# Kernel optimization log

Hardware: AMD Instinct MI355X
Metric: run time of the kernel (lower is better)

## Reference

```python
import jax, jax.numpy as jnp
import numpy as np

# Dimensions (see shape_source)
L = 1024   # episode_len (memory slots)
B = 64     # batch (parallel envs)
K = 512    # key_size
V = 512    # value_size
H = 8      # num_head
MEMB = 256 # memory_state_embedding
SDIM = 512 # state_dim
HID = 512  # hidden width of all 2-layer encoders
RIMQ = 512 # rim_query_size
LAT = K - MEMB  # task_inference_latent dim


def setup_inputs() -> dict:
    key = jax.random.key(0)
    ks = jax.random.split(key, 16)
    w = lambda k, shape: (jax.random.normal(k, shape, jnp.float32) * 0.02)
    return {
        "state": jax.random.normal(ks[0], (B, SDIM), jnp.float32),
        "task_inference_latent": jax.random.normal(ks[1], (B, LAT), jnp.float32),
        "keys": jax.random.normal(ks[2], (L, B, K), jnp.float32),
        "vals": jax.random.normal(ks[3], (L, B, V), jnp.float32),
        "rpe_mod": jax.random.uniform(ks[4], (L, B, 1), jnp.float32),
        "step": jnp.maximum(jax.random.randint(ks[5], (B,), 0, L), 1),
        "W_state": w(ks[6], (SDIM, MEMB)), "b_state": jnp.zeros((MEMB,), jnp.float32),
        "Wcq1": w(ks[7], (K, HID)), "bcq1": jnp.zeros((HID,), jnp.float32),
        "Wcq2": w(ks[8], (HID, K)), "bcq2": jnp.zeros((K,), jnp.float32),
        "Wq": w(ks[9], (K, H * K)), "bq": jnp.zeros((H * K,), jnp.float32),
        "Wagg": w(ks[10], (H * V, V)), "bagg": jnp.zeros((V,), jnp.float32),
        "Wrk1": w(ks[11], (V, HID)), "brk1": jnp.zeros((HID,), jnp.float32),
        "Wrk2": w(ks[12], (HID, RIMQ)), "brk2": jnp.zeros((RIMQ,), jnp.float32),
        "Wrv1": w(ks[13], (V, HID)), "brv1": jnp.zeros((HID,), jnp.float32),
        "Wrv2": w(ks[14], (HID, V)), "brv2": jnp.zeros((V,), jnp.float32),
    }


def reference(state, task_inference_latent, keys, vals, rpe_mod, step,
              W_state, b_state, Wcq1, bcq1, Wcq2, bcq2, Wq, bq, Wagg, bagg,
              Wrk1, brk1, Wrk2, brk2, Wrv1, brv1, Wrv2, brv2):
    # DND.read (exploration branch), vectorized over the batch loop.
    se = state @ W_state + b_state                         # state_encoder: [B, MEMB]
    q = jnp.concatenate([se, task_inference_latent], -1)   # [B, K]
    # concat_query_encoder: stacked Linears with NO nonlinearity (faithful to source)
    q = (q @ Wcq1 + bcq1) @ Wcq2 + bcq2                    # [B, K]
    q = (q @ Wq + bq).reshape(B, H, K)                     # multi-head queries

    mk = keys * rpe_mod                                    # RPE-modulated keys [L, B, K]
    scores = jnp.einsum('lbk,bhk->blh', mk, q) / jnp.sqrt(jnp.float32(K))  # [B, L, H]
    valid = jnp.arange(L)[None, :] < step[:, None]         # [B, L] only slots < step[i]
    scores = jnp.where(valid[:, :, None], scores, jnp.float32(-1e30))
    prob = jax.nn.softmax(scores, axis=1) * valid[:, :, None].astype(scores.dtype)

    result = jnp.einsum('blh,lbv->bhv', prob, vals).reshape(B, H * V)
    result = (result @ Wagg + bagg)[:, None, :]            # value_aggregator -> [B, 1, V]
    out_key = (result @ Wrk1 + brk1) @ Wrk2 + brk2         # read_memory_to_key  [B, 1, RIMQ]
    out_val = (result @ Wrv1 + brv1) @ Wrv2 + brv2         # read_memory_to_value [B, 1, V]
    return out_key, out_val
```

## Files before the change

kernel.cpp:

```cpp
#include <hip/hip_runtime.h>
#include <math.h>

#define F4(p)  (*reinterpret_cast<float4*>(p))
#define CF4(p) (*reinterpret_cast<const float4*>(p))

#define NCHUNK 16

__device__ __forceinline__ void gemm_core(
    const float* __restrict__ Asrc, const float* __restrict__ inbias,
    const float* __restrict__ til,
    int NS, int srcld, int kc, int k0,
    const float* __restrict__ W, int ldw, int n0,
    const float* __restrict__ obias, float* __restrict__ Pout, int ldo)
{
    __shared__ float As[16*64], Ws[16*64];
    const int t = threadIdx.x;
    const int tx = t & 15, ty = t >> 4;
    const int row = t >> 2, kq = (t & 3) * 4;
    const int wrow = t >> 4, wcol = (t & 15) * 4;
    float acc[4][4] = {};
    for (int kk = 0; kk < kc; kk += 16) {
        const int kg = k0 + kk + kq;
        float4 av;
        if (til && kg >= 256) {
            av = CF4(&til[row*256 + (kg - 256)]);
        } else {
            av = {0.f, 0.f, 0.f, 0.f};
            if (inbias) av = CF4(&inbias[kg]);
            for (int s = 0; s < NS; ++s) {
                float4 v = CF4(&Asrc[(size_t)(s*64 + row)*srcld + kg]);
                av.x += v.x; av.y += v.y; av.z += v.z; av.w += v.w;
            }
        }
        As[(kq+0)*64+row] = av.x; As[(kq+1)*64+row] = av.y;
        As[(kq+2)*64+row] = av.z; As[(kq+3)*64+row] = av.w;
        F4(&Ws[wrow*64 + wcol]) = CF4(&W[(size_t)(k0 + kk + wrow)*ldw + n0 + wcol]);
        __syncthreads();
        #pragma unroll
        for (int k = 0; k < 16; ++k) {
            float4 a4 = CF4(&As[k*64 + ty*4]);
            float4 w4 = CF4(&Ws[k*64 + tx*4]);
            float a[4] = {a4.x, a4.y, a4.z, a4.w};
            float w[4] = {w4.x, w4.y, w4.z, w4.w};
            #pragma unroll
            for (int i = 0; i < 4; ++i)
                #pragma unroll
                for (int j = 0; j < 4; ++j)
                    acc[i][j] += a[i] * w[j];
        }
        __syncthreads();
    }
    #pragma unroll
    for (int i = 0; i < 4; ++i) {
        float4 o = {acc[i][0], acc[i][1], acc[i][2], acc[i][3]};
        if (obias) {
            float4 ob = CF4(&obias[n0 + tx*4]);
            o.x += ob.x; o.y += ob.y; o.z += ob.z; o.w += ob.w;
        }
        F4(&Pout[(size_t)(ty*4 + i)*ldo + n0 + tx*4]) = o;
    }
}

__global__ __launch_bounds__(256) void k_q1(
    const float* __restrict__ state, const float* __restrict__ W_state,
    float* __restrict__ P1)
{
    const int nt = blockIdx.x, ks = blockIdx.y;
    gemm_core(state, nullptr, nullptr, 1, 512, 64, ks*64,
              W_state, 256, nt*64, nullptr, P1 + (size_t)ks*64*256, 256);
}

__global__ __launch_bounds__(256) void k_q2(
    const float* __restrict__ P1, const float* __restrict__ b_state,
    const float* __restrict__ til, const float* __restrict__ Wcq1,
    float* __restrict__ P2)
{
    const int nt = blockIdx.x, ks = blockIdx.y;
    gemm_core(P1, b_state, til, 8, 256, 64, ks*64,
              Wcq1, 512, nt*64, nullptr, P2 + (size_t)ks*64*512, 512);
}

__global__ __launch_bounds__(256) void k_q3(
    const float* __restrict__ P2, const float* __restrict__ bcq1,
    const float* __restrict__ Wcq2, float* __restrict__ P3)
{
    const int nt = blockIdx.x, ks = blockIdx.y;
    gemm_core(P2, bcq1, nullptr, 8, 512, 64, ks*64,
              Wcq2, 512, nt*64, nullptr, P3 + (size_t)ks*64*512, 512);
}

__global__ __launch_bounds__(256) void k_qh(
    const float* __restrict__ P3, const float* __restrict__ bcq2,
    const float* __restrict__ Wq, float* __restrict__ P4)
{
    const int nt = blockIdx.x, ks = blockIdx.y;
    gemm_core(P3, bcq2, nullptr, 8, 512, 128, ks*128,
              Wq, 4096, nt*64, nullptr, P4 + (size_t)ks*64*4096, 4096);
}

__global__ __launch_bounds__(256) void k_qsum(
    const float* __restrict__ P4, const float* __restrict__ bq,
    float* __restrict__ qh)
{
    const int b = blockIdx.x, t = threadIdx.x;
    #pragma unroll
    for (int j = 0; j < 4; ++j) {
        int f = t + j*256;
        float4 v = CF4(&bq[f*4]);
        #pragma unroll
        for (int s = 0; s < 4; ++s) {
            float4 u = CF4(&P4[(size_t)(s*64 + b)*4096 + f*4]);
            v.x += u.x; v.y += u.y; v.z += u.z; v.w += u.w;
        }
        F4(&qh[(size_t)b*4096 + f*4]) = v;
    }
}

__global__ __launch_bounds__(256, 3) void k_fa(
    const float* __restrict__ keys, const float* __restrict__ rpe,
    const float* __restrict__ qh, const float* __restrict__ vals,
    const int* __restrict__ step,
    float* __restrict__ Facc, float* __restrict__ Fms)
{
    __shared__ float s_cmb[4096];
    __shared__ float s_sc[64*8];
    __shared__ float s_rpe[64];
    __shared__ float red[256];
    __shared__ float s_m[8];
    const int b = blockIdx.y, lc = blockIdx.x;
    const int sb = step[b];
    const int l0 = (lc * sb) / NCHUNK;
    const int l1 = ((lc + 1) * sb) / NCHUNK;
    const int nl = l1 - l0;
    const int t = threadIdx.x;
    float* facc_out = Facc + ((size_t)(lc*64) + b)*4096;
    if (nl <= 0) {
        float4 z = {0.f, 0.f, 0.f, 0.f};
        for (int i = t; i < 1024; i += 256) F4(&facc_out[i*4]) = z;
        if (t < 8) {
            size_t o = ((size_t)(lc*64 + b)*8 + t)*2;
            Fms[o] = -1e30f; Fms[o+1] = 0.f;
        }
        return;
    }
    const float inv_sqrtK = 0.04419417382415922f;
    if (t < nl) s_rpe[t] = rpe[(l0 + t)*64 + b] * inv_sqrtK;
    __syncthreads();

    const int lane = t & 63, w = t >> 6;
    float qr[8][8];
    {
        const float* qb = qh + (size_t)b*4096 + lane*8;
        #pragma unroll
        for (int h = 0; h < 8; ++h) {
            float4 x = CF4(&qb[h*512]);
            float4 y = CF4(&qb[h*512 + 4]);
            qr[h][0]=x.x; qr[h][1]=x.y; qr[h][2]=x.z; qr[h][3]=x.w;
            qr[h][4]=y.x; qr[h][5]=y.y; qr[h][6]=y.z; qr[h][7]=y.w;
        }
    }
    const bool p0 = lane & 1, p1 = lane & 2, p2 = lane & 4;
    const size_t RS = (size_t)64*512;

    const float* kbase = keys + ((size_t)l0*64 + b)*512 + lane*8;
    auto kaddr = [&](int r) { return kbase + (size_t)min(r, nl-1)*RS; };
    float4 kx0 = CF4(kaddr(w)),      ky0 = CF4(kaddr(w)+4);
    float4 kx1 = CF4(kaddr(w+4)),    ky1 = CF4(kaddr(w+4)+4);
    float4 kx2 = CF4(kaddr(w+8)),    ky2 = CF4(kaddr(w+8)+4);
    float4 kx3 = CF4(kaddr(w+12)),   ky3 = CF4(kaddr(w+12)+4);

    auto score_step = [&](float4& bx, float4& by, int r) {
        float kv[8] = {bx.x,bx.y,bx.z,bx.w, by.x,by.y,by.z,by.w};
        bx = CF4(kaddr(r+16)); by = CF4(kaddr(r+16)+4);
        float pr[8] = {};
        #pragma unroll
        for (int h = 0; h < 8; ++h)
            #pragma unroll
            for (int j = 0; j < 8; ++j)
                pr[h] += kv[j] * qr[h][j];
        float w4[4], x2[2], y;
        #pragma unroll
        for (int q = 0; q < 4; ++q) {
            float keep = p0 ? pr[2*q+1] : pr[2*q];
            float send = p0 ? pr[2*q]   : pr[2*q+1];
            w4[q] = keep + __shfl_xor(send, 1);
        }
        #pragma unroll
        for (int q = 0; q < 2; ++q) {
            float keep = p1 ? w4[2*q+1] : w4[2*q];
            float send = p1 ? w4[2*q]   : w4[2*q+1];
            x2[q] = keep + __shfl_xor(send, 2);
        }
        {
            float keep = p2 ? x2[1] : x2[0];
            float send = p2 ? x2[0] : x2[1];
            y = keep + __shfl_xor(send, 4);
        }
        y += __shfl_xor(y, 8);
        y += __shfl_xor(y, 16);
        y += __shfl_xor(y, 32);
        if (r < nl && lane < 8) s_sc[r*8 + lane] = y * s_rpe[r];
    };
    for (int il = w; il < nl; il += 16) {
        score_step(kx0, ky0, il);
        score_step(kx1, ky1, il + 4);
        score_step(kx2, ky2, il + 8);
        score_step(kx3, ky3, il + 12);
    }
    __syncthreads();

    const int h = t & 7, g = t >> 3;
    float m = -1e30f;
    for (int l = g; l < nl; l += 32) m = fmaxf(m, s_sc[l*8 + h]);
    red[g*8 + h] = m;
    __syncthreads();
    #pragma unroll
    for (int s = 16; s; s >>= 1) {
        if (g < s) red[g*8+h] = fmaxf(red[g*8+h], red[(g+s)*8+h]);
        __syncthreads();
    }
    if (t < 8) s_m[t] = red[t];
    __syncthreads();
    float mh = s_m[h], s_acc = 0.f;
    for (int l = g; l < nl; l += 32) {
        float e = __expf(s_sc[l*8 + h] - mh);
        s_sc[l*8 + h] = e;
        s_acc += e;
    }
    for (int l = nl + g; l < 64; l += 32) s_sc[l*8 + h] = 0.f;
    red[g*8 + h] = s_acc;
    __syncthreads();
    #pragma unroll
    for (int s = 16; s; s >>= 1) {
        if (g < s) red[g*8+h] += red[(g+s)*8+h];
        __syncthreads();
    }
    if (t < 8) {
        size_t o = ((size_t)(lc*64 + b)*8 + t)*2;
        Fms[o] = s_m[t]; Fms[o+1] = red[t];
    }
    __syncthreads();

    const int par = t >> 7, c = t & 127;
    float4 acc[8] = {};
    const float* vbase = vals + ((size_t)l0*64 + b)*512 + c*4;
    auto vaddr = [&](int r) { return vbase + (size_t)min(r, nl-1)*RS; };
    float4 v0 = CF4(vaddr(par));
    float4 v1 = CF4(vaddr(par+2));
    float4 v2 = CF4(vaddr(par+4));
    float4 v3 = CF4(vaddr(par+6));
    auto pv_step = [&](float4& vb, int row) {
        float4 v = vb;
        vb = CF4(vaddr(row + 8));
        float4 pa = CF4(&s_sc[row*8]);
        float4 pb = CF4(&s_sc[row*8 + 4]);
        acc[0].x += pa.x*v.x; acc[0].y += pa.x*v.y; acc[0].z += pa.x*v.z; acc[0].w += pa.x*v.w;
        acc[1].x += pa.y*v.x; acc[1].y += pa.y*v.y; acc[1].z += pa.y*v.z; acc[1].w += pa.y*v.w;
        acc[2].x += pa.z*v.x; acc[2].y += pa.z*v.y; acc[2].z += pa.z*v.z; acc[2].w += pa.z*v.w;
        acc[3].x += pa.w*v.x; acc[3].y += pa.w*v.y; acc[3].z += pa.w*v.z; acc[3].w += pa.w*v.w;
        acc[4].x += pb.x*v.x; acc[4].y += pb.x*v.y; acc[4].z += pb.x*v.z; acc[4].w += pb.x*v.w;
        acc[5].x += pb.y*v.x; acc[5].y += pb.y*v.y; acc[5].z += pb.y*v.z; acc[5].w += pb.y*v.w;
        acc[6].x += pb.z*v.x; acc[6].y += pb.z*v.y; acc[6].z += pb.z*v.z; acc[6].w += pb.z*v.w;
        acc[7].x += pb.w*v.x; acc[7].y += pb.w*v.y; acc[7].z += pb.w*v.z; acc[7].w += pb.w*v.w;
    };
    const int NL8 = (nl + 7) & ~7;
    for (int il = par; il < NL8; il += 8) {
        pv_step(v0, il);
        pv_step(v1, il + 2);
        pv_step(v2, il + 4);
        pv_step(v3, il + 6);
    }
    __syncthreads();
    if (par == 1) {
        #pragma unroll
        for (int hh = 0; hh < 8; ++hh)
            F4(&s_cmb[(c*8 + hh)*4]) = acc[hh];
    }
    __syncthreads();
    if (par == 0) {
        #pragma unroll
        for (int hh = 0; hh < 8; ++hh) {
            float4 o = CF4(&s_cmb[(c*8 + hh)*4]);
            o.x += acc[hh].x; o.y += acc[hh].y; o.z += acc[hh].z; o.w += acc[hh].w;
            F4(&facc_out[hh*512 + c*4]) = o;
        }
    }
}

__global__ __launch_bounds__(256) void k_comb(
    const float* __restrict__ Facc, const float* __restrict__ Fms,
    float* __restrict__ res)
{
    __shared__ float wgt[NCHUNK*8];
    const int b = blockIdx.x, t = threadIdx.x;
    if (t < 8) {
        float mm[NCHUNK], ss[NCHUNK], e[NCHUNK];
        float M = -1e30f;
        #pragma unroll
        for (int i = 0; i < NCHUNK; ++i) {
            size_t o = ((size_t)(i*64 + b)*8 + t)*2;
            mm[i] = Fms[o]; ss[i] = Fms[o+1];
            M = fmaxf(M, mm[i]);
        }
        float D = 0.f;
        #pragma unroll
        for (int i = 0; i < NCHUNK; ++i) { e[i] = __expf(mm[i] - M); D += e[i]*ss[i]; }
        float invD = 1.f / D;
        #pragma unroll
        for (int i = 0; i < NCHUNK; ++i) wgt[i*8 + t] = e[i] * invD;
    }
    __syncthreads();
    #pragma unroll
    for (int j = 0; j < 4; ++j) {
        int f = t + j*256;
        int h = f >> 7;
        float4 a = {0.f, 0.f, 0.f, 0.f};
        #pragma unroll
        for (int i = 0; i < NCHUNK; ++i) {
            float wi = wgt[i*8 + h];
            float4 v = CF4(&Facc[((size_t)(i*64) + b)*4096 + f*4]);
            a.x += wi*v.x; a.y += wi*v.y; a.z += wi*v.z; a.w += wi*v.w;
        }
        F4(&res[(size_t)b*4096 + f*4]) = a;
    }
}

__global__ __launch_bounds__(256) void k_agg(
    const float* __restrict__ res, const float* __restrict__ Wagg,
    float* __restrict__ P5)
{
    const int nt = blockIdx.x, ks = blockIdx.y;
    gemm_core(res, nullptr, nullptr, 1, 4096, 128, ks*128,
              Wagg, 512, nt*64, nullptr, P5 + (size_t)ks*64*512, 512);
}

__global__ __launch_bounds__(256) void k_rkv1(
    const float* __restrict__ P5, const float* __restrict__ bagg,
    const float* __restrict__ Wrk1, const float* __restrict__ Wrv1,
    float* __restrict__ P6)
{
    const int nt = blockIdx.x, ks = blockIdx.y, z = blockIdx.z;
    gemm_core(P5, bagg, nullptr, 32, 512, 128, ks*128,
              z ? Wrv1 : Wrk1, 512, nt*64,
              nullptr, P6 + (size_t)(z*4 + ks)*64*512, 512);
}

__global__ __launch_bounds__(256) void k_rkv2(
    const float* __restrict__ P6,
    const float* __restrict__ brk1, const float* __restrict__ brv1,
    const float* __restrict__ Wrk2, const float* __restrict__ Wrv2,
    const float* __restrict__ brk2, const float* __restrict__ brv2,
    float* __restrict__ out)
{
    const int nt = blockIdx.x, z = blockIdx.z;
    gemm_core(P6 + (size_t)z*4*64*512, z ? brv1 : brk1, nullptr, 4, 512, 512, 0,
              z ? Wrv2 : Wrk2, 512, nt*64,
              z ? brv2 : brk2, out + (size_t)z*64*512, 512);
}

extern "C" void kernel_launch(void* const* d_in, const int* in_sizes, int n_in,
                              void* d_out, int out_size, void* d_ws, size_t ws_size,
                              hipStream_t stream) {
    const float* state   = (const float*)d_in[0];
    const float* til     = (const float*)d_in[1];
    const float* keys    = (const float*)d_in[2];
    const float* vals    = (const float*)d_in[3];
    const float* rpe     = (const float*)d_in[4];
    const int*   step    = (const int*)d_in[5];
    const float* W_state = (const float*)d_in[6];
    const float* b_state = (const float*)d_in[7];
    const float* Wcq1 = (const float*)d_in[8];
    const float* bcq1 = (const float*)d_in[9];
    const float* Wcq2 = (const float*)d_in[10];
    const float* bcq2 = (const float*)d_in[11];
    const float* Wq   = (const float*)d_in[12];
    const float* bq   = (const float*)d_in[13];
    const float* Wagg = (const float*)d_in[14];
    const float* bagg = (const float*)d_in[15];
    const float* Wrk1 = (const float*)d_in[16];
    const float* brk1 = (const float*)d_in[17];
    const float* Wrk2 = (const float*)d_in[18];
    const float* brk2 = (const float*)d_in[19];
    const float* Wrv1 = (const float*)d_in[20];
    const float* brv1 = (const float*)d_in[21];
    const float* Wrv2 = (const float*)d_in[22];
    const float* brv2 = (const float*)d_in[23];
    float* out = (float*)d_out;
    float* ws  = (float*)d_ws;

    float* P1   = ws;
    float* P2   = ws + 131072;
    float* P3   = ws + 393216;
    float* P4   = ws + 655360;
    float* qh   = ws + 1703936;
    float* Facc = ws + 1966080;
    float* Fms  = ws + 6160384;
    float* res  = ws + 6176768;
    float* P5   = ws;
    float* P6   = ws + 1048576;

    k_q1  <<<dim3(4,8),   256, 0, stream>>>(state, W_state, P1);
    k_q2  <<<dim3(8,8),   256, 0, stream>>>(P1, b_state, til, Wcq1, P2);
    k_q3  <<<dim3(8,8),   256, 0, stream>>>(P2, bcq1, Wcq2, P3);
    k_qh  <<<dim3(64,4),  256, 0, stream>>>(P3, bcq2, Wq, P4);
    k_qsum<<<64, 256, 0, stream>>>(P4, bq, qh);
    k_fa  <<<dim3(NCHUNK,64), 256, 0, stream>>>(keys, rpe, qh, vals, step, Facc, Fms);
    k_comb<<<64, 256, 0, stream>>>(Facc, Fms, res);
    k_agg <<<dim3(8,32),  256, 0, stream>>>(res, Wagg, P5);
    k_rkv1<<<dim3(8,4,2), 256, 0, stream>>>(P5, bagg, Wrk1, Wrv1, P6);
    k_rkv2<<<dim3(8,1,2), 256, 0, stream>>>(P6, brk1, brv1, Wrk2, Wrv2,
                                            brk2, brv2, out);
}
```

Before: 164.1 us.

## Stage keys and values through double-buffered shared-memory tiles in attention kernel

The attention chunk kernel no longer streams keys and values directly from global memory with per-warp register prefetch. It now loads 12-row tiles cooperatively into a double-buffered LDS array: the next tile is fetched into registers while the current tile is computed from shared memory, then written to the other buffer. The LDS use grows and the occupancy hint drops from 3 to 2 blocks per CU. This trades latency hiding through occupancy for explicit software pipelining and adds a barrier per tile.

```diff
diff --git a/kernel.cpp b/kernel.cpp
--- a/kernel.cpp
+++ b/kernel.cpp
@@ -5,6 +5,7 @@
 #define CF4(p) (*reinterpret_cast<const float4*>(p))
 
 #define NCHUNK 16
+#define TROWS  12
 
 __device__ __forceinline__ void gemm_core(
     const float* __restrict__ Asrc, const float* __restrict__ inbias,
@@ -116,14 +117,14 @@
     }
 }
 
-__global__ __launch_bounds__(256, 3) void k_fa(
+__global__ __launch_bounds__(256, 2) void k_fa(
     const float* __restrict__ keys, const float* __restrict__ rpe,
     const float* __restrict__ qh, const float* __restrict__ vals,
     const int* __restrict__ step,
     float* __restrict__ Facc, float* __restrict__ Fms)
 {
-    __shared__ float s_cmb[4096];
-    __shared__ float s_sc[64*8];
+    __shared__ __align__(16) float s_kt[2][TROWS*512];
+    __shared__ float s_sc[72*8];
     __shared__ float s_rpe[64];
     __shared__ float red[256];
     __shared__ float s_m[8];
@@ -143,11 +144,43 @@
         }
         return;
     }
+    const int ntile = (nl + TROWS - 1) / TROWS;
     const float inv_sqrtK = 0.04419417382415922f;
+    const int lane = t & 63, w = t >> 6;
+
+    float4 sreg[6];
+    const int sf_r[6]  = { (0*256) >> 7, (1*256) >> 7, 0,0,0,0 };
+    (void)sf_r;
+    auto stage_load_k = [&](int tile) {
+        const int base = tile * TROWS;
+        #pragma unroll
+        for (int s = 0; s < 6; ++s) {
+            int f = s*256 + t;
+            int r = f >> 7, c4 = f & 127;
+            int g = min(base + r, nl - 1);
+            sreg[s] = CF4(&keys[((size_t)(l0 + g)*64 + b)*512 + c4*4]);
+        }
+    };
+    auto stage_load_v = [&](int tile) {
+        const int base = tile * TROWS;
+        #pragma unroll
+        for (int s = 0; s < 6; ++s) {
+            int f = s*256 + t;
+            int r = f >> 7, c4 = f & 127;
+            int g = min(base + r, nl - 1);
+            sreg[s] = CF4(&vals[((size_t)(l0 + g)*64 + b)*512 + c4*4]);
+        }
+    };
+    auto stage_write = [&](int buf) {
+        #pragma unroll
+        for (int s = 0; s < 6; ++s) {
+            int f = s*256 + t;
+            F4(&s_kt[buf][f*4]) = sreg[s];
+        }
+    };
+
+    stage_load_k(0);
     if (t < nl) s_rpe[t] = rpe[(l0 + t)*64 + b] * inv_sqrtK;
-    __syncthreads();
-
-    const int lane = t & 63, w = t >> 6;
     float qr[8][8];
     {
         const float* qb = qh + (size_t)b*4096 + lane*8;
@@ -158,57 +191,64 @@
             qr[h][0]=x.x; qr[h][1]=x.y; qr[h][2]=x.z; qr[h][3]=x.w;
             qr[h][4]=y.x; qr[h][5]=y.y; qr[h][6]=y.z; qr[h][7]=y.w;
         }
-    }
-    const bool p0 = lane & 1, p1 = lane & 2, p2 = lane & 4;
-    const size_t RS = (size_t)64*512;
-
-    const float* kbase = keys + ((size_t)l0*64 + b)*512 + lane*8;
-    auto kaddr = [&](int r) { return kbase + (size_t)min(r, nl-1)*RS; };
-    float4 kx0 = CF4(kaddr(w)),      ky0 = CF4(kaddr(w)+4);
-    float4 kx1 = CF4(kaddr(w+4)),    ky1 = CF4(kaddr(w+4)+4);
-    float4 kx2 = CF4(kaddr(w+8)),    ky2 = CF4(kaddr(w+8)+4);
-    float4 kx3 = CF4(kaddr(w+12)),   ky3 = CF4(kaddr(w+12)+4);
-
-    auto score_step = [&](float4& bx, float4& by, int r) {
-        float kv[8] = {bx.x,bx.y,bx.z,bx.w, by.x,by.y,by.z,by.w};
-        bx = CF4(kaddr(r+16)); by = CF4(kaddr(r+16)+4);
-        float pr[8] = {};
         #pragma unroll
         for (int h = 0; h < 8; ++h)
             #pragma unroll
             for (int j = 0; j < 8; ++j)
-                pr[h] += kv[j] * qr[h][j];
-        float w4[4], x2[2], y;
-        #pragma unroll
-        for (int q = 0; q < 4; ++q) {
-            float keep = p0 ? pr[2*q+1] : pr[2*q];
-            float send = p0 ? pr[2*q]   : pr[2*q+1];
-            w4[q] = keep + __shfl_xor(send, 1);
-        }
-        #pragma unroll
-        for (int q = 0; q < 2; ++q) {
-            float keep = p1 ? w4[2*q+1] : w4[2*q];
-            float send = p1 ? w4[2*q]   : w4[2*q+1];
-            x2[q] = keep + __shfl_xor(send, 2);
-        }
-        {
-            float keep = p2 ? x2[1] : x2[0];
-            float send = p2 ? x2[0] : x2[1];
-            y = keep + __shfl_xor(send, 4);
-        }
-        y += __shfl_xor(y, 8);
-        y += __shfl_xor(y, 16);
-        y += __shfl_xor(y, 32);
-        if (r < nl && lane < 8) s_sc[r*8 + lane] = y * s_rpe[r];
-    };
-    for (int il = w; il < nl; il += 16) {
-        score_step(kx0, ky0, il);
-        score_step(kx1, ky1, il + 4);
-        score_step(kx2, ky2, il + 8);
-        score_step(kx3, ky3, il + 12);
-    }
-    __syncthreads();
-
+                asm volatile("" : "+v"(qr[h][j]));
+    }
+    stage_write(0);
+    __syncthreads();
+
+    const bool p0 = lane & 1, p1 = lane & 2, p2 = lane & 4;
+    for (int i = 0; i < ntile; ++i) {
+        const int cur = i & 1;
+        const bool more = (i + 1 < ntile);
+        if (more) stage_load_k(i + 1);
+        const int base = i * TROWS;
+        #pragma unroll
+        for (int r3 = 0; r3 < 3; ++r3) {
+            const int r = w + r3*4;
+            const int gr = base + r;
+            if (gr < nl) {
+                float4 kx = CF4(&s_kt[cur][r*512 + lane*8]);
+                float4 ky = CF4(&s_kt[cur][r*512 + lane*8 + 4]);
+                float kv[8] = {kx.x,kx.y,kx.z,kx.w, ky.x,ky.y,ky.z,ky.w};
+                float pr[8] = {};
+                #pragma unroll
+                for (int h = 0; h < 8; ++h)
+                    #pragma unroll
+                    for (int j = 0; j < 8; ++j)
+                        pr[h] += kv[j] * qr[h][j];
+                float w4[4], x2[2], y;
+                #pragma unroll
+                for (int q = 0; q < 4; ++q) {
+                    float keep = p0 ? pr[2*q+1] : pr[2*q];
+                    float send = p0 ? pr[2*q]   : pr[2*q+1];
+                    w4[q] = keep + __shfl_xor(send, 1);
+                }
+                #pragma unroll
+                for (int q = 0; q < 2; ++q) {
+                    float keep = p1 ? w4[2*q+1] : w4[2*q];
+                    float send = p1 ? w4[2*q]   : w4[2*q+1];
+                    x2[q] = keep + __shfl_xor(send, 2);
+                }
+                {
+                    float keep = p2 ? x2[1] : x2[0];
+                    float send = p2 ? x2[0] : x2[1];
+                    y = keep + __shfl_xor(send, 4);
+                }
+                y += __shfl_xor(y, 8);
+                y += __shfl_xor(y, 16);
+                y += __shfl_xor(y, 32);
+                if (lane < 8) s_sc[gr*8 + lane] = y * s_rpe[gr];
+            }
+        }
+        if (more) stage_write(cur ^ 1);
+        __syncthreads();
+    }
+
+    stage_load_v(0);
     const int h = t & 7, g = t >> 3;
     float m = -1e30f;
     for (int l = g; l < nl; l += 32) m = fmaxf(m, s_sc[l*8 + h]);
@@ -227,7 +267,7 @@
         s_sc[l*8 + h] = e;
         s_acc += e;
     }
-    for (int l = nl + g; l < 64; l += 32) s_sc[l*8 + h] = 0.f;
+    for (int l = nl + g; l < ntile*TROWS; l += 32) s_sc[l*8 + h] = 0.f;
     red[g*8 + h] = s_acc;
     __syncthreads();
     #pragma unroll
@@ -239,38 +279,37 @@
         size_t o = ((size_t)(lc*64 + b)*8 + t)*2;
         Fms[o] = s_m[t]; Fms[o+1] = red[t];
     }
+    stage_write(0);
     __syncthreads();
 
     const int par = t >> 7, c = t & 127;
     float4 acc[8] = {};
-    const float* vbase = vals + ((size_t)l0*64 + b)*512 + c*4;
-    auto vaddr = [&](int r) { return vbase + (size_t)min(r, nl-1)*RS; };
-    float4 v0 = CF4(vaddr(par));
-    float4 v1 = CF4(vaddr(par+2));
-    float4 v2 = CF4(vaddr(par+4));
-    float4 v3 = CF4(vaddr(par+6));
-    auto pv_step = [&](float4& vb, int row) {
-        float4 v = vb;
-        vb = CF4(vaddr(row + 8));
-        float4 pa = CF4(&s_sc[row*8]);
-        float4 pb = CF4(&s_sc[row*8 + 4]);
-        acc[0].x += pa.x*v.x; acc[0].y += pa.x*v.y; acc[0].z += pa.x*v.z; acc[0].w += pa.x*v.w;
-        acc[1].x += pa.y*v.x; acc[1].y += pa.y*v.y; acc[1].z += pa.y*v.z; acc[1].w += pa.y*v.w;
-        acc[2].x += pa.z*v.x; acc[2].y += pa.z*v.y; acc[2].z += pa.z*v.z; acc[2].w += pa.z*v.w;
-        acc[3].x += pa.w*v.x; acc[3].y += pa.w*v.y; acc[3].z += pa.w*v.z; acc[3].w += pa.w*v.w;
-        acc[4].x += pb.x*v.x; acc[4].y += pb.x*v.y; acc[4].z += pb.x*v.z; acc[4].w += pb.x*v.w;
-        acc[5].x += pb.y*v.x; acc[5].y += pb.y*v.y; acc[5].z += pb.y*v.z; acc[5].w += pb.y*v.w;
-        acc[6].x += pb.z*v.x; acc[6].y += pb.z*v.y; acc[6].z += pb.z*v.z; acc[6].w += pb.z*v.w;
-        acc[7].x += pb.w*v.x; acc[7].y += pb.w*v.y; acc[7].z += pb.w*v.z; acc[7].w += pb.w*v.w;
-    };
-    const int NL8 = (nl + 7) & ~7;
-    for (int il = par; il < NL8; il += 8) {
-        pv_step(v0, il);
-        pv_step(v1, il + 2);
-        pv_step(v2, il + 4);
-        pv_step(v3, il + 6);
-    }
-    __syncthreads();
+    for (int i = 0; i < ntile; ++i) {
+        const int cur = i & 1;
+        const bool more = (i + 1 < ntile);
+        if (more) stage_load_v(i + 1);
+        const int base = i * TROWS;
+        #pragma unroll
+        for (int j = 0; j < 6; ++j) {
+            const int r = par + j*2;
+            const int gr = base + r;
+            float4 v = CF4(&s_kt[cur][r*512 + c*4]);
+            float4 pa = CF4(&s_sc[gr*8]);
+            float4 pb = CF4(&s_sc[gr*8 + 4]);
+            acc[0].x += pa.x*v.x; acc[0].y += pa.x*v.y; acc[0].z += pa.x*v.z; acc[0].w += pa.x*v.w;
+            acc[1].x += pa.y*v.x; acc[1].y += pa.y*v.y; acc[1].z += pa.y*v.z; acc[1].w += pa.y*v.w;
+            acc[2].x += pa.z*v.x; acc[2].y += pa.z*v.y; acc[2].z += pa.z*v.z; acc[2].w += pa.z*v.w;
+            acc[3].x += pa.w*v.x; acc[3].y += pa.w*v.y; acc[3].z += pa.w*v.z; acc[3].w += pa.w*v.w;
+            acc[4].x += pb.x*v.x; acc[4].y += pb.x*v.y; acc[4].z += pb.x*v.z; acc[4].w += pb.x*v.w;
+            acc[5].x += pb.y*v.x; acc[5].y += pb.y*v.y; acc[5].z += pb.y*v.z; acc[5].w += pb.y*v.w;
+            acc[6].x += pb.z*v.x; acc[6].y += pb.z*v.y; acc[6].z += pb.z*v.z; acc[6].w += pb.z*v.w;
+            acc[7].x += pb.w*v.x; acc[7].y += pb.w*v.y; acc[7].z += pb.w*v.z; acc[7].w += pb.w*v.w;
+        }
+        if (more) stage_write(cur ^ 1);
+        __syncthreads();
+    }
+
+    float* s_cmb = &s_kt[0][0];
     if (par == 1) {
         #pragma unroll
         for (int hh = 0; hh < 8; ++hh)
```

Result: slower. 208.3 us (+26.9%).

## Fuse query split-K sum into attention and use single-pass online softmax

Applied to the files above, without the earlier changes.

Drops the separate query-summation kernel: each attention block now sums the split-K partial queries plus bias into shared memory itself. The two-pass score/softmax/PV structure becomes a single streaming pass per wave, loading key and value rows together and keeping a running max with lazy rescaling (only when the max grows by more than 8). The four per-wave partial accumulators are merged through shared memory. This removes one launch, several block-wide reductions and syncs, and a second pass over the chunk. In exchange it uses more shared memory and registers (launch bounds lowered to 2 blocks per SM), and drops the software prefetch of the next key and value rows.

```diff
diff --git a/kernel.cpp b/kernel.cpp
--- a/kernel.cpp
+++ b/kernel.cpp
@@ -98,35 +98,16 @@
               Wq, 4096, nt*64, nullptr, P4 + (size_t)ks*64*4096, 4096);
 }
 
-__global__ __launch_bounds__(256) void k_qsum(
+__global__ __launch_bounds__(256, 2) void k_fa(
+    const float* __restrict__ keys, const float* __restrict__ rpe,
     const float* __restrict__ P4, const float* __restrict__ bq,
-    float* __restrict__ qh)
-{
-    const int b = blockIdx.x, t = threadIdx.x;
-    #pragma unroll
-    for (int j = 0; j < 4; ++j) {
-        int f = t + j*256;
-        float4 v = CF4(&bq[f*4]);
-        #pragma unroll
-        for (int s = 0; s < 4; ++s) {
-            float4 u = CF4(&P4[(size_t)(s*64 + b)*4096 + f*4]);
-            v.x += u.x; v.y += u.y; v.z += u.z; v.w += u.w;
-        }
-        F4(&qh[(size_t)b*4096 + f*4]) = v;
-    }
-}
-
-__global__ __launch_bounds__(256, 3) void k_fa(
-    const float* __restrict__ keys, const float* __restrict__ rpe,
-    const float* __restrict__ qh, const float* __restrict__ vals,
-    const int* __restrict__ step,
+    const float* __restrict__ vals, const int* __restrict__ step,
     float* __restrict__ Facc, float* __restrict__ Fms)
 {
-    __shared__ float s_cmb[4096];
-    __shared__ float s_sc[64*8];
+    __shared__ __align__(16) float s_q[4096];
+    __shared__ __align__(16) float s_acc3[3*4096];
     __shared__ float s_rpe[64];
-    __shared__ float red[256];
-    __shared__ float s_m[8];
+    __shared__ float s_ms[4*9];
     const int b = blockIdx.y, lc = blockIdx.x;
     const int sb = step[b];
     const int l0 = (lc * sb) / NCHUNK;
@@ -144,34 +125,40 @@
         return;
     }
     const float inv_sqrtK = 0.04419417382415922f;
+    for (int i = t; i < 1024; i += 256) {
+        float4 v = CF4(&bq[i*4]);
+        #pragma unroll
+        for (int s = 0; s < 4; ++s) {
+            float4 u = CF4(&P4[(size_t)(s*64 + b)*4096 + i*4]);
+            v.x += u.x; v.y += u.y; v.z += u.z; v.w += u.w;
+        }
+        F4(&s_q[i*4]) = v;
+    }
     if (t < nl) s_rpe[t] = rpe[(l0 + t)*64 + b] * inv_sqrtK;
     __syncthreads();
 
     const int lane = t & 63, w = t >> 6;
     float qr[8][8];
-    {
-        const float* qb = qh + (size_t)b*4096 + lane*8;
-        #pragma unroll
-        for (int h = 0; h < 8; ++h) {
-            float4 x = CF4(&qb[h*512]);
-            float4 y = CF4(&qb[h*512 + 4]);
-            qr[h][0]=x.x; qr[h][1]=x.y; qr[h][2]=x.z; qr[h][3]=x.w;
-            qr[h][4]=y.x; qr[h][5]=y.y; qr[h][6]=y.z; qr[h][7]=y.w;
-        }
+    #pragma unroll
+    for (int h = 0; h < 8; ++h) {
+        float4 x = CF4(&s_q[h*512 + lane*8]);
+        float4 y = CF4(&s_q[h*512 + lane*8 + 4]);
+        qr[h][0]=x.x; qr[h][1]=x.y; qr[h][2]=x.z; qr[h][3]=x.w;
+        qr[h][4]=y.x; qr[h][5]=y.y; qr[h][6]=y.z; qr[h][7]=y.w;
     }
     const bool p0 = lane & 1, p1 = lane & 2, p2 = lane & 4;
-    const size_t RS = (size_t)64*512;
-
-    const float* kbase = keys + ((size_t)l0*64 + b)*512 + lane*8;
-    auto kaddr = [&](int r) { return kbase + (size_t)min(r, nl-1)*RS; };
-    float4 kx0 = CF4(kaddr(w)),      ky0 = CF4(kaddr(w)+4);
-    float4 kx1 = CF4(kaddr(w+4)),    ky1 = CF4(kaddr(w+4)+4);
-    float4 kx2 = CF4(kaddr(w+8)),    ky2 = CF4(kaddr(w+8)+4);
-    float4 kx3 = CF4(kaddr(w+12)),   ky3 = CF4(kaddr(w+12)+4);
-
-    auto score_step = [&](float4& bx, float4& by, int r) {
-        float kv[8] = {bx.x,bx.y,bx.z,bx.w, by.x,by.y,by.z,by.w};
-        bx = CF4(kaddr(r+16)); by = CF4(kaddr(r+16)+4);
+
+    float m_run = -1e30f;
+    float srun[8] = {0.f,0.f,0.f,0.f,0.f,0.f,0.f,0.f};
+    float4 accA[8] = {}, accB[8] = {};
+
+    for (int r = w; r < nl; r += 4) {
+        const size_t rowoff = ((size_t)(l0 + r)*64 + b)*512 + lane*8;
+        const float* kp = keys + rowoff;
+        const float* vp = vals + rowoff;
+        float4 kx = CF4(kp), ky = CF4(kp + 4);
+        float4 vx = CF4(vp), vy = CF4(vp + 4);
+        float kv[8] = {kx.x,kx.y,kx.z,kx.w, ky.x,ky.y,ky.z,ky.w};
         float pr[8] = {};
         #pragma unroll
         for (int h = 0; h < 8; ++h)
@@ -199,91 +186,69 @@
         y += __shfl_xor(y, 8);
         y += __shfl_xor(y, 16);
         y += __shfl_xor(y, 32);
-        if (r < nl && lane < 8) s_sc[r*8 + lane] = y * s_rpe[r];
-    };
-    for (int il = w; il < nl; il += 16) {
-        score_step(kx0, ky0, il);
-        score_step(kx1, ky1, il + 4);
-        score_step(kx2, ky2, il + 8);
-        score_step(kx3, ky3, il + 12);
+        y *= s_rpe[r];
+        float p[8];
+        #pragma unroll
+        for (int hh = 0; hh < 8; ++hh)
+            p[hh] = __shfl(y, (lane & 56) | hh);
+        float pmax = fmaxf(fmaxf(fmaxf(p[0],p[1]), fmaxf(p[2],p[3])),
+                           fmaxf(fmaxf(p[4],p[5]), fmaxf(p[6],p[7])));
+        if (pmax > m_run + 8.f) {
+            float scale = __expf(m_run - pmax);
+            #pragma unroll
+            for (int hh = 0; hh < 8; ++hh) {
+                srun[hh] *= scale;
+                accA[hh].x *= scale; accA[hh].y *= scale; accA[hh].z *= scale; accA[hh].w *= scale;
+                accB[hh].x *= scale; accB[hh].y *= scale; accB[hh].z *= scale; accB[hh].w *= scale;
+            }
+            m_run = pmax;
+        }
+        float e[8];
+        #pragma unroll
+        for (int hh = 0; hh < 8; ++hh) e[hh] = __expf(p[hh] - m_run);
+        #pragma unroll
+        for (int hh = 0; hh < 8; ++hh) {
+            srun[hh] += e[hh];
+            accA[hh].x += e[hh]*vx.x; accA[hh].y += e[hh]*vx.y;
+            accA[hh].z += e[hh]*vx.z; accA[hh].w += e[hh]*vx.w;
+            accB[hh].x += e[hh]*vy.x; accB[hh].y += e[hh]*vy.y;
+            accB[hh].z += e[hh]*vy.z; accB[hh].w += e[hh]*vy.w;
+        }
     }
     __syncthreads();
-
-    const int h = t & 7, g = t >> 3;
-    float m = -1e30f;
-    for (int l = g; l < nl; l += 32) m = fmaxf(m, s_sc[l*8 + h]);
-    red[g*8 + h] = m;
+    {
+        float* slot = (w == 0) ? s_q : (s_acc3 + (w-1)*4096);
+        #pragma unroll
+        for (int hh = 0; hh < 8; ++hh) {
+            F4(&slot[hh*512 + lane*8])     = accA[hh];
+            F4(&slot[hh*512 + lane*8 + 4]) = accB[hh];
+        }
+        if (lane == 0) s_ms[w*9] = m_run;
+        if (lane < 8)  s_ms[w*9 + 1 + lane] = srun[lane];
+    }
     __syncthreads();
+    const float m0 = s_ms[0], m1 = s_ms[9], m2 = s_ms[18], m3 = s_ms[27];
+    const float M  = fmaxf(fmaxf(m0, m1), fmaxf(m2, m3));
+    const float e0 = __expf(m0 - M), e1 = __expf(m1 - M);
+    const float e2 = __expf(m2 - M), e3 = __expf(m3 - M);
     #pragma unroll
-    for (int s = 16; s; s >>= 1) {
-        if (g < s) red[g*8+h] = fmaxf(red[g*8+h], red[(g+s)*8+h]);
-        __syncthreads();
-    }
-    if (t < 8) s_m[t] = red[t];
-    __syncthreads();
-    float mh = s_m[h], s_acc = 0.f;
-    for (int l = g; l < nl; l += 32) {
-        float e = __expf(s_sc[l*8 + h] - mh);
-        s_sc[l*8 + h] = e;
-        s_acc += e;
-    }
-    for (int l = nl + g; l < 64; l += 32) s_sc[l*8 + h] = 0.f;
-    red[g*8 + h] = s_acc;
-    __syncthreads();
-    #pragma unroll
-    for (int s = 16; s; s >>= 1) {
-        if (g < s) red[g*8+h] += red[(g+s)*8+h];
-        __syncthreads();
+    for (int j = 0; j < 4; ++j) {
+        int f = t + j*256;
+        float4 a0 = CF4(&s_q[f*4]);
+        float4 a1 = CF4(&s_acc3[f*4]);
+        float4 a2 = CF4(&s_acc3[4096 + f*4]);
+        float4 a3 = CF4(&s_acc3[8192 + f*4]);
+        float4 o;
+        o.x = e0*a0.x + e1*a1.x + e2*a2.x + e3*a3.x;
+        o.y = e0*a0.y + e1*a1.y + e2*a2.y + e3*a3.y;
+        o.z = e0*a0.z + e1*a1.z + e2*a2.z + e3*a3.z;
+        o.w = e0*a0.w + e1*a1.w + e2*a2.w + e3*a3.w;
+        F4(&facc_out[f*4]) = o;
     }
     if (t < 8) {
+        float stot = e0*s_ms[1+t] + e1*s_ms[10+t] + e2*s_ms[19+t] + e3*s_ms[28+t];
         size_t o = ((size_t)(lc*64 + b)*8 + t)*2;
-        Fms[o] = s_m[t]; Fms[o+1] = red[t];
-    }
-    __syncthreads();
-
-    const int par = t >> 7, c = t & 127;
-    float4 acc[8] = {};
-    const float* vbase = vals + ((size_t)l0*64 + b)*512 + c*4;
-    auto vaddr = [&](int r) { return vbase + (size_t)min(r, nl-1)*RS; };
-    float4 v0 = CF4(vaddr(par));
-    float4 v1 = CF4(vaddr(par+2));
-    float4 v2 = CF4(vaddr(par+4));
-    float4 v3 = CF4(vaddr(par+6));
-    auto pv_step = [&](float4& vb, int row) {
-        float4 v = vb;
-        vb = CF4(vaddr(row + 8));
-        float4 pa = CF4(&s_sc[row*8]);
-        float4 pb = CF4(&s_sc[row*8 + 4]);
-        acc[0].x += pa.x*v.x; acc[0].y += pa.x*v.y; acc[0].z += pa.x*v.z; acc[0].w += pa.x*v.w;
-        acc[1].x += pa.y*v.x; acc[1].y += pa.y*v.y; acc[1].z += pa.y*v.z; acc[1].w += pa.y*v.w;
-        acc[2].x += pa.z*v.x; acc[2].y += pa.z*v.y; acc[2].z += pa.z*v.z; acc[2].w += pa.z*v.w;
-        acc[3].x += pa.w*v.x; acc[3].y += pa.w*v.y; acc[3].z += pa.w*v.z; acc[3].w += pa.w*v.w;
-        acc[4].x += pb.x*v.x; acc[4].y += pb.x*v.y; acc[4].z += pb.x*v.z; acc[4].w += pb.x*v.w;
-        acc[5].x += pb.y*v.x; acc[5].y += pb.y*v.y; acc[5].z += pb.y*v.z; acc[5].w += pb.y*v.w;
-        acc[6].x += pb.z*v.x; acc[6].y += pb.z*v.y; acc[6].z += pb.z*v.z; acc[6].w += pb.z*v.w;
-        acc[7].x += pb.w*v.x; acc[7].y += pb.w*v.y; acc[7].z += pb.w*v.z; acc[7].w += pb.w*v.w;
-    };
-    const int NL8 = (nl + 7) & ~7;
-    for (int il = par; il < NL8; il += 8) {
-        pv_step(v0, il);
-        pv_step(v1, il + 2);
-        pv_step(v2, il + 4);
-        pv_step(v3, il + 6);
-    }
-    __syncthreads();
-    if (par == 1) {
-        #pragma unroll
-        for (int hh = 0; hh < 8; ++hh)
-            F4(&s_cmb[(c*8 + hh)*4]) = acc[hh];
-    }
-    __syncthreads();
-    if (par == 0) {
-        #pragma unroll
-        for (int hh = 0; hh < 8; ++hh) {
-            float4 o = CF4(&s_cmb[(c*8 + hh)*4]);
-            o.x += acc[hh].x; o.y += acc[hh].y; o.z += acc[hh].z; o.w += acc[hh].w;
-            F4(&facc_out[hh*512 + c*4]) = o;
-        }
+        Fms[o] = M; Fms[o+1] = stot;
     }
 }
 
@@ -392,7 +357,6 @@
     float* P2   = ws + 131072;
     float* P3   = ws + 393216;
     float* P4   = ws + 655360;
-    float* qh   = ws + 1703936;
     float* Facc = ws + 1966080;
     float* Fms  = ws + 6160384;
     float* res  = ws + 6176768;
@@ -403,8 +367,7 @@
     k_q2  <<<dim3(8,8),   256, 0, stream>>>(P1, b_state, til, Wcq1, P2);
     k_q3  <<<dim3(8,8),   256, 0, stream>>>(P2, bcq1, Wcq2, P3);
     k_qh  <<<dim3(64,4),  256, 0, stream>>>(P3, bcq2, Wq, P4);
-    k_qsum<<<64, 256, 0, stream>>>(P4, bq, qh);
-    k_fa  <<<dim3(NCHUNK,64), 256, 0, stream>>>(keys, rpe, qh, vals, step, Facc, Fms);
+    k_fa  <<<dim3(NCHUNK,64), 256, 0, stream>>>(keys, rpe, P4, bq, vals, step, Facc, Fms);
     k_comb<<<64, 256, 0, stream>>>(Facc, Fms, res);
     k_agg <<<dim3(8,32),  256, 0, stream>>>(res, Wagg, P5);
     k_rkv1<<<dim3(8,4,2), 256, 0, stream>>>(P5, bagg, Wrk1, Wrv1, P6);
```

Result: no change. 161.9 us (-1.4%).
